# Optimization experiments

Hardware: AMD Instinct MI355X
Metric: run time of the kernel (lower is better)

## Reference

```python
import jax, jax.numpy as jnp
import numpy as np

N_NODES = 100000
N_EDGES = 1600000
N_IN = 8
N_PRE = 32
C = 128
N_LAYERS = 8


def _lin(key, fan_in, fan_out):
    kw, kb = jax.random.split(key)
    s = 1.0 / np.sqrt(fan_in).astype(np.float32)
    W = jax.random.uniform(kw, (fan_in, fan_out), minval=-s, maxval=s, dtype=jnp.float32)
    b = jax.random.uniform(kb, (fan_out,), minval=-s, maxval=s, dtype=jnp.float32)
    return W, b


def setup_inputs() -> dict:
    key = jax.random.key(0)
    ks = jax.random.split(key, 9)
    x = jax.random.normal(ks[0], (N_NODES, N_IN), dtype=jnp.float32)
    edge_index = jax.random.randint(ks[1], (2, N_EDGES), 0, N_NODES, dtype=jnp.int32)
    Wp, bp = _lin(ks[2], N_IN, N_PRE)      # preproc
    W1, b1 = _lin(ks[3], N_PRE, C)         # fc_input_1 (node_identity)
    W2, b2 = _lin(ks[4], N_PRE, C)         # fc_input_2
    Wg, bg = _lin(ks[5], C, C)             # tied GCNConv weight/bias
    Wd, bd = _lin(ks[6], 2 * C, C)         # tied dense fusion
    Wf1, bf1 = _lin(ks[7], 2 * C, C)       # final_fc1
    Wf2, bf2 = _lin(ks[8], C, 2)           # final_fc2
    return {"x": x, "edge_index": edge_index, "Wp": Wp, "bp": bp, "W1": W1, "b1": b1,
            "W2": W2, "b2": b2, "Wg": Wg, "bg": bg, "Wd": Wd, "bd": bd,
            "Wf1": Wf1, "bf1": bf1, "Wf2": Wf2, "bf2": bf2}


def _gcn(h, Wg, bg, src, dst):
    # PyG GCNConv: add self-loops, norm = deg^-1/2[src] * deg^-1/2[dst].
    # Norm factorizes, so scale at node level instead of per edge.
    hw = h @ Wg                                                  # [N, C]
    deg = jnp.zeros((N_NODES,), jnp.float32).at[dst].add(1.0) + 1.0  # +1 self-loop
    dis = jax.lax.rsqrt(deg)                                     # deg^-1/2
    hs = hw * dis[:, None]
    agg = jax.ops.segment_sum(hs[src], dst, num_segments=N_NODES)
    return (agg + hs) * dis[:, None] + bg                        # hs term = self-loop (deg^-1 * hw)


def reference(x, edge_index, Wp, bp, W1, b1, W2, b2, Wg, bg, Wd, bd, Wf1, bf1, Wf2, bf2):
    src, dst = edge_index[0], edge_index[1]
    h0 = x @ Wp + bp                       # preproc_activation = none
    ni = jax.nn.relu(h0 @ W1 + b1)         # node_identity
    h = jax.nn.relu(h0 @ W2 + b2)
    for _ in range(N_LAYERS):              # tied gnn layers; dropout is identity (inference)
        g = jax.nn.relu(_gcn(h, Wg, bg, src, dst))
        h = jax.nn.relu(jnp.concatenate([ni, g], axis=1) @ Wd + bd)
    h = jax.nn.relu(jnp.concatenate([ni, h], axis=1) @ Wf1 + bf1)
    return h @ Wf2 + bf2                   # output_activation never applied in forward
```

## Files before the change

### kernel.cpp

```cpp
#include <hip/hip_runtime.h>

#define N_NODES 100000
#define N_EDGES 1600000
#define NB 391
#define NTASK (N_NODES / 16)
#define COLPAD (N_EDGES + 7 * N_NODES + 64)

typedef unsigned short ushort_t;
typedef __attribute__((ext_vector_type(8))) short bf16x8;
typedef __attribute__((ext_vector_type(4))) float f32x4;

__device__ __forceinline__ float bf2f(unsigned short u) {
    union { unsigned u; float f; } x; x.u = ((unsigned)u) << 16; return x.f;
}
__device__ __forceinline__ unsigned short f2bf(float f) {
    union { float f; unsigned u; } x; x.f = f;
    unsigned r = x.u + 0x7fffu + ((x.u >> 16) & 1u);
    return (unsigned short)(r >> 16);
}

__global__ void k_zero(unsigned* p, int n) {
    int i = blockIdx.x * 256 + threadIdx.x;
    if (i < n) p[i] = 0u;
}

__global__ void k_filld(unsigned* p) {
    int i = blockIdx.x * 256 + threadIdx.x;
    if (i < COLPAD) p[i] = (unsigned)N_NODES;
}

__global__ void k_deg(const int* __restrict__ dst, unsigned* __restrict__ cnt) {
    int e = blockIdx.x * 256 + threadIdx.x;
    if (e < N_EDGES) atomicAdd(&cnt[dst[e]], 1u);
}

__global__ void k_dis(const unsigned* __restrict__ cnt, float* __restrict__ dis,
                      float* __restrict__ sdeg) {
    int i = blockIdx.x * 256 + threadIdx.x;
    if (i < N_NODES) {
        float d = (float)cnt[i] + 1.0f;
        float s = sqrtf(d);
        sdeg[i] = s;
        dis[i] = 1.0f / s;
    }
}

__global__ void __launch_bounds__(256) k_bsum(const unsigned* __restrict__ cnt,
                                              unsigned* __restrict__ bsum) {
    __shared__ unsigned sh[256];
    int i = blockIdx.x * 256 + threadIdx.x;
    sh[threadIdx.x] = (i < N_NODES) ? ((cnt[i] + 7u) & ~7u) : 0u;
    __syncthreads();
    for (int off = 128; off > 0; off >>= 1) {
        if (threadIdx.x < off) sh[threadIdx.x] += sh[threadIdx.x + off];
        __syncthreads();
    }
    if (threadIdx.x == 0) bsum[blockIdx.x] = sh[0];
}

__global__ void __launch_bounds__(512) k_bscan(unsigned* __restrict__ bsum) {
    __shared__ unsigned sh[512];
    int t = threadIdx.x;
    unsigned v = (t < NB) ? bsum[t] : 0u;
    sh[t] = v;
    __syncthreads();
    for (int off = 1; off < 512; off <<= 1) {
        unsigned u = (t >= off) ? sh[t - off] : 0u;
        __syncthreads();
        sh[t] += u;
        __syncthreads();
    }
    if (t < NB) bsum[t] = sh[t] - v;
}

__global__ void __launch_bounds__(256) k_apply(const unsigned* __restrict__ cnt,
                                               const unsigned* __restrict__ bsum,
                                               unsigned* __restrict__ prow,
                                               unsigned* __restrict__ cur) {
    __shared__ unsigned sh[256];
    int i = blockIdx.x * 256 + threadIdx.x;
    int t = threadIdx.x;
    unsigned v = (i < N_NODES) ? ((cnt[i] + 7u) & ~7u) : 0u;
    sh[t] = v;
    __syncthreads();
    for (int off = 1; off < 256; off <<= 1) {
        unsigned u = (t >= off) ? sh[t - off] : 0u;
        __syncthreads();
        sh[t] += u;
        __syncthreads();
    }
    if (i < N_NODES) {
        prow[i] = bsum[blockIdx.x] + sh[t] - v;
        cur[i] = 0u;
    }
    if (i == N_NODES - 1) prow[N_NODES] = bsum[blockIdx.x] + sh[t];
}

__global__ void k_fill(const int* __restrict__ src, const int* __restrict__ dst,
                       const unsigned* __restrict__ prow, unsigned* __restrict__ cur,
                       unsigned* __restrict__ colp) {
    int e = blockIdx.x * 256 + threadIdx.x;
    if (e < N_EDGES) {
        int d = dst[e];
        unsigned pos = prow[d] + atomicAdd(&cur[d], 1u);
        colp[pos] = (unsigned)src[e];
    }
}

__global__ void __launch_bounds__(256) k_sort(const unsigned* __restrict__ prow,
                                              unsigned* __restrict__ colp) {
    int i = blockIdx.x * 256 + threadIdx.x;
    if (i >= N_NODES) return;
    unsigned b = prow[i], e = prow[i + 1];
    for (unsigned j = b + 1; j < e; ++j) {
        unsigned v = colp[j];
        unsigned k = j;
        while (k > b && colp[k - 1] > v) { colp[k] = colp[k - 1]; --k; }
        colp[k] = v;
    }
}

__global__ void k_dummy(ushort_t* hdA, ushort_t* hdB) {
    int t = threadIdx.x;
    if (t < 128) hdA[(size_t)N_NODES * 128 + t] = 0;
    else hdB[(size_t)N_NODES * 128 + (t - 128)] = 0;
}

__global__ void k_tr(const float* __restrict__ Wd, const float* __restrict__ Wf1,
                     const float* __restrict__ Wg, ushort_t* __restrict__ WT) {
    const float* srcs[5] = {Wd, Wf1, Wg, Wd + 128 * 128, Wf1 + 128 * 128};
    const float* S = srcs[blockIdx.x];
    ushort_t* Dhi = WT + (size_t)(2 * blockIdx.x) * 16384;
    ushort_t* Dlo = Dhi + 16384;
    for (int i = threadIdx.x; i < 128 * 128; i += blockDim.x) {
        int n = i >> 7, k = i & 127;
        float w = S[k * 128 + n];
        unsigned short h = f2bf(w);
        Dhi[n * 128 + k] = h;
        Dlo[n * 128 + k] = f2bf(w - bf2f(h));
    }
}

__global__ void __launch_bounds__(128) k_pre1(
    const float* __restrict__ x, const float* __restrict__ Wp,
    const float* __restrict__ bp, const float* __restrict__ W1,
    const float* __restrict__ b1, const float* __restrict__ W2,
    const float* __restrict__ b2, const float* __restrict__ dis,
    ushort_t* __restrict__ ni, ushort_t* __restrict__ hd) {
    __shared__ float h0s[4][32];
    int j = threadIdx.x;
    long n0 = (long)blockIdx.x * 4;
    {
        int nn = j >> 5, c = j & 31;
        float acc = bp[c];
#pragma unroll
        for (int k = 0; k < 8; ++k)
            acc += x[(n0 + nn) * 8 + k] * Wp[k * 32 + c];
        h0s[nn][c] = acc;
    }
    __syncthreads();
    float ni_a[4], h1_a[4];
    float bb1 = b1[j], bb2 = b2[j];
#pragma unroll
    for (int m = 0; m < 4; ++m) { ni_a[m] = bb1; h1_a[m] = bb2; }
    for (int cc = 0; cc < 32; ++cc) {
        float w1 = W1[cc * 128 + j];
        float w2 = W2[cc * 128 + j];
#pragma unroll
        for (int m = 0; m < 4; ++m) {
            float h0v = h0s[m][cc];
            ni_a[m] += h0v * w1;
            h1_a[m] += h0v * w2;
        }
    }
#pragma unroll
    for (int m = 0; m < 4; ++m) {
        long node = n0 + m;
        ni[node * 128 + j] = f2bf(fmaxf(ni_a[m], 0.f));
        hd[node * 128 + j] = f2bf(fmaxf(h1_a[m], 0.f) * dis[node]);
    }
}

__device__ __forceinline__ void load_split_frags(const float* __restrict__ p,
                                                 bf16x8* ahi, bf16x8* alo) {
#pragma unroll
    for (int kc = 0; kc < 4; ++kc) {
        const float* q = p + kc * 32;
#pragma unroll
        for (int j = 0; j < 8; ++j) {
            float f = q[j];
            unsigned short h = f2bf(f);
            ahi[kc][j] = (short)h;
            alo[kc][j] = (short)f2bf(f - bf2f(h));
        }
    }
}

__device__ __forceinline__ void mfma_tiles(const bf16x8* ahi, const bf16x8* alo,
                                           const ushort_t* __restrict__ WThi,
                                           const ushort_t* __restrict__ WTlo,
                                           int r16, int q, f32x4* acc) {
#pragma unroll
    for (int t = 0; t < 8; ++t) {
        const ushort_t* bh = WThi + (t * 16 + r16) * 128 + q * 8;
        const ushort_t* bl = WTlo + (t * 16 + r16) * 128 + q * 8;
#pragma unroll
        for (int kc = 0; kc < 4; ++kc) {
            bf16x8 bhv = *(const bf16x8*)(bh + kc * 32);
            bf16x8 blv = *(const bf16x8*)(bl + kc * 32);
            acc[t] = __builtin_amdgcn_mfma_f32_16x16x32_bf16(alo[kc], bhv, acc[t], 0, 0, 0);
            acc[t] = __builtin_amdgcn_mfma_f32_16x16x32_bf16(ahi[kc], blv, acc[t], 0, 0, 0);
            acc[t] = __builtin_amdgcn_mfma_f32_16x16x32_bf16(ahi[kc], bhv, acc[t], 0, 0, 0);
        }
    }
}

__global__ void __launch_bounds__(256) k_niw(
    const ushort_t* __restrict__ in,
    const ushort_t* __restrict__ hiA, const ushort_t* __restrict__ loA,
    const float* __restrict__ biasA, ushort_t* __restrict__ outA,
    const ushort_t* __restrict__ hiB, const ushort_t* __restrict__ loB,
    const float* __restrict__ biasB, ushort_t* __restrict__ outB) {
    int task = blockIdx.x * 4 + (threadIdx.x >> 6);
    if (task >= NTASK) return;
    int lane = threadIdx.x & 63;
    int q = lane >> 4, r16 = lane & 15;
    long base = (long)task * 16;

    bf16x8 a[4];
    const ushort_t* arow = in + (base + r16) * 128 + q * 8;
#pragma unroll
    for (int kc = 0; kc < 4; ++kc) a[kc] = *(const bf16x8*)(arow + kc * 32);

    f32x4 accA[8], accB[8];
#pragma unroll
    for (int t = 0; t < 8; ++t) { accA[t] = {0.f, 0.f, 0.f, 0.f}; accB[t] = {0.f, 0.f, 0.f, 0.f}; }
#pragma unroll
    for (int t = 0; t < 8; ++t) {
        const ushort_t* bhA = hiA + (t * 16 + r16) * 128 + q * 8;
        const ushort_t* blA = loA + (t * 16 + r16) * 128 + q * 8;
        const ushort_t* bhB = hiB + (t * 16 + r16) * 128 + q * 8;
        const ushort_t* blB = loB + (t * 16 + r16) * 128 + q * 8;
#pragma unroll
        for (int kc = 0; kc < 4; ++kc) {
            accA[t] = __builtin_amdgcn_mfma_f32_16x16x32_bf16(a[kc], *(const bf16x8*)(blA + kc * 32), accA[t], 0, 0, 0);
            accA[t] = __builtin_amdgcn_mfma_f32_16x16x32_bf16(a[kc], *(const bf16x8*)(bhA + kc * 32), accA[t], 0, 0, 0);
            accB[t] = __builtin_amdgcn_mfma_f32_16x16x32_bf16(a[kc], *(const bf16x8*)(blB + kc * 32), accB[t], 0, 0, 0);
            accB[t] = __builtin_amdgcn_mfma_f32_16x16x32_bf16(a[kc], *(const bf16x8*)(bhB + kc * 32), accB[t], 0, 0, 0);
        }
    }
#pragma unroll
    for (int t = 0; t < 8; ++t) {
        int n = t * 16 + r16;
        float bvA = biasA[n], bvB = biasB[n];
#pragma unroll
        for (int r = 0; r < 4; ++r) {
            long node = base + q * 4 + r;
            outA[node * 128 + n] = f2bf(accA[t][r] + bvA);
            outB[node * 128 + n] = f2bf(accB[t][r] + bvB);
        }
    }
}

__device__ __forceinline__ void acc8(uint4 w, float* a) {
    a[0] += __uint_as_float(w.x << 16);
    a[1] += __uint_as_float(w.x & 0xffff0000u);
    a[2] += __uint_as_float(w.y << 16);
    a[3] += __uint_as_float(w.y & 0xffff0000u);
    a[4] += __uint_as_float(w.z << 16);
    a[5] += __uint_as_float(w.z & 0xffff0000u);
    a[6] += __uint_as_float(w.w << 16);
    a[7] += __uint_as_float(w.w & 0xffff0000u);
}

__device__ __forceinline__ void gather8(uint4* G, uint4 c0, uint4 c1,
                                        const uint4* __restrict__ h4, int l) {
    G[0] = h4[(long)c0.x * 16 + l];
    G[1] = h4[(long)c0.y * 16 + l];
    G[2] = h4[(long)c0.z * 16 + l];
    G[3] = h4[(long)c0.w * 16 + l];
    G[4] = h4[(long)c1.x * 16 + l];
    G[5] = h4[(long)c1.y * 16 + l];
    G[6] = h4[(long)c1.z * 16 + l];
    G[7] = h4[(long)c1.w * 16 + l];
}

__device__ __forceinline__ void accbatch(const uint4* G, float* a) {
#pragma unroll
    for (int j = 0; j < 8; ++j) acc8(G[j], a);
}

__global__ void __launch_bounds__(256, 4) k_fused(
    const unsigned* __restrict__ prow, const unsigned* __restrict__ colp,
    const ushort_t* __restrict__ hd_in,
    const ushort_t* __restrict__ hi_wg, const ushort_t* __restrict__ lo_wg,
    const float* __restrict__ bg,
    const ushort_t* __restrict__ hi_wd, const ushort_t* __restrict__ lo_wd,
    const ushort_t* __restrict__ niWd, const float* __restrict__ dis,
    ushort_t* __restrict__ hd_out) {
    __shared__ float gsh[4][16 * 132];
    int wid = threadIdx.x >> 6;
    int lane = threadIdx.x & 63;
    int task = blockIdx.x * 4 + wid;
    if (task >= NTASK) return;
    long base = (long)task * 16;
    float* gw = gsh[wid];
    const uint4* h4 = (const uint4*)hd_in;

    int g = lane >> 4;
    int l = lane & 15;

#pragma unroll 1
    for (int i = 0; i < 4; ++i) {
        int m = g * 4 + i;
        long node = base + m;
        float a[8] = {0.f, 0.f, 0.f, 0.f, 0.f, 0.f, 0.f, 0.f};
        uint4 own = h4[node * 16 + l];
        unsigned t0 = prow[node];
        int nb = (int)((prow[node + 1] - t0) >> 3);
        acc8(own, a);
        if (nb > 0) {
            const uint4* cp = (const uint4*)(colp + t0);
            uint4 cX0 = cp[0], cX1 = cp[1];
            uint4 cY0 = cp[2], cY1 = cp[3];
            cp += 4;
            uint4 GA[8], GB[8];
            gather8(GA, cX0, cX1, h4, l);
            int k = 0;
            for (; k + 2 < nb; k += 2) {
                cX0 = cp[0]; cX1 = cp[1];
                gather8(GB, cY0, cY1, h4, l);
                accbatch(GA, a);
                cY0 = cp[2]; cY1 = cp[3];
                cp += 4;
                gather8(GA, cX0, cX1, h4, l);
                accbatch(GB, a);
            }
            if (nb - k == 2) {
                gather8(GB, cY0, cY1, h4, l);
                accbatch(GA, a);
                accbatch(GB, a);
            } else {
                accbatch(GA, a);
            }
        }
        float* dstp = gw + m * 132 + 8 * l;
        *(float4*)dstp = make_float4(a[0], a[1], a[2], a[3]);
        *(float4*)(dstp + 4) = make_float4(a[4], a[5], a[6], a[7]);
    }

    int q = lane >> 4, r16 = lane & 15;
    bf16x8 ahi[4], alo[4];
    load_split_frags(gw + r16 * 132 + q * 8, ahi, alo);

    f32x4 acc[8];
#pragma unroll
    for (int t = 0; t < 8; ++t) acc[t] = {0.f, 0.f, 0.f, 0.f};
    mfma_tiles(ahi, alo, hi_wg, lo_wg, r16, q, acc);

    float sc[4];
#pragma unroll
    for (int r = 0; r < 4; ++r) sc[r] = dis[base + q * 4 + r];

#pragma unroll
    for (int t = 0; t < 8; ++t) {
        int n = t * 16 + r16;
        float bv = bg[n];
#pragma unroll
        for (int r = 0; r < 4; ++r) {
            int m = q * 4 + r;
            gw[m * 132 + n] = fmaxf(acc[t][r] * sc[r] + bv, 0.f);
        }
    }

    load_split_frags(gw + r16 * 132 + q * 8, ahi, alo);
#pragma unroll
    for (int t = 0; t < 8; ++t) acc[t] = {0.f, 0.f, 0.f, 0.f};
    mfma_tiles(ahi, alo, hi_wd, lo_wd, r16, q, acc);

#pragma unroll
    for (int t = 0; t < 8; ++t) {
        int n = t * 16 + r16;
#pragma unroll
        for (int r = 0; r < 4; ++r) {
            long node = base + q * 4 + r;
            float nv = bf2f(niWd[node * 128 + n]);
            hd_out[node * 128 + n] = f2bf(fmaxf(acc[t][r] + nv, 0.f) * sc[r]);
        }
    }
}

__global__ void __launch_bounds__(256) k_fin(
    const ushort_t* __restrict__ in, const ushort_t* __restrict__ WThi,
    const ushort_t* __restrict__ WTlo, const ushort_t* __restrict__ niWf,
    const float* __restrict__ sdeg, float* __restrict__ out) {
    int task = blockIdx.x * 4 + (threadIdx.x >> 6);
    if (task >= NTASK) return;
    int lane = threadIdx.x & 63;
    int q = lane >> 4, r16 = lane & 15;
    long base = (long)task * 16;

    bf16x8 a[4];
    const ushort_t* arow = in + (base + r16) * 128 + q * 8;
#pragma unroll
    for (int kc = 0; kc < 4; ++kc) a[kc] = *(const bf16x8*)(arow + kc * 32);

    f32x4 acc[8];
#pragma unroll
    for (int t = 0; t < 8; ++t) acc[t] = {0.f, 0.f, 0.f, 0.f};
#pragma unroll
    for (int t = 0; t < 8; ++t) {
        const ushort_t* bh = WThi + (t * 16 + r16) * 128 + q * 8;
        const ushort_t* bl = WTlo + (t * 16 + r16) * 128 + q * 8;
#pragma unroll
        for (int kc = 0; kc < 4; ++kc) {
            bf16x8 bhv = *(const bf16x8*)(bh + kc * 32);
            bf16x8 blv = *(const bf16x8*)(bl + kc * 32);
            acc[t] = __builtin_amdgcn_mfma_f32_16x16x32_bf16(a[kc], blv, acc[t], 0, 0, 0);
            acc[t] = __builtin_amdgcn_mfma_f32_16x16x32_bf16(a[kc], bhv, acc[t], 0, 0, 0);
        }
    }

    float sc[4];
#pragma unroll
    for (int r = 0; r < 4; ++r) sc[r] = sdeg[base + q * 4 + r];
#pragma unroll
    for (int t = 0; t < 8; ++t) {
        int n = t * 16 + r16;
#pragma unroll
        for (int r = 0; r < 4; ++r) {
            long node = base + q * 4 + r;
            float nv = bf2f(niWf[node * 128 + n]);
            out[node * 128 + n] = fmaxf(acc[t][r] * sc[r] + nv, 0.f);
        }
    }
}

__global__ void __launch_bounds__(256) k_fc2(const float* __restrict__ hf,
                                             const float* __restrict__ Wf2,
                                             const float* __restrict__ bf2v,
                                             float* __restrict__ out) {
    int node = blockIdx.x * 4 + (threadIdx.x >> 6);
    if (node >= N_NODES) return;
    int lane = threadIdx.x & 63;
    float2 hv = ((const float2*)hf)[(long)node * 64 + lane];
    float4 wv = *(const float4*)(Wf2 + lane * 4);
    float p0 = hv.x * wv.x + hv.y * wv.z;
    float p1 = hv.x * wv.y + hv.y * wv.w;
    for (int o = 32; o > 0; o >>= 1) {
        p0 += __shfl_down(p0, o, 64);
        p1 += __shfl_down(p1, o, 64);
    }
    if (lane == 0) {
        float2 r; r.x = p0 + bf2v[0]; r.y = p1 + bf2v[1];
        ((float2*)out)[node] = r;
    }
}

extern "C" void kernel_launch(void* const* d_in, const int* in_sizes, int n_in,
                              void* d_out, int out_size, void* d_ws, size_t ws_size,
                              hipStream_t stream) {
    const float* x    = (const float*)d_in[0];
    const int* ei     = (const int*)d_in[1];
    const float* Wp   = (const float*)d_in[2];
    const float* bp   = (const float*)d_in[3];
    const float* W1   = (const float*)d_in[4];
    const float* b1   = (const float*)d_in[5];
    const float* W2   = (const float*)d_in[6];
    const float* b2   = (const float*)d_in[7];
    const float* Wg   = (const float*)d_in[8];
    const float* bg   = (const float*)d_in[9];
    const float* Wd   = (const float*)d_in[10];
    const float* bd   = (const float*)d_in[11];
    const float* Wf1  = (const float*)d_in[12];
    const float* bf1  = (const float*)d_in[13];
    const float* Wf2  = (const float*)d_in[14];
    const float* bf2v = (const float*)d_in[15];

    char* w = (char*)d_ws;
    auto carve = [&](size_t bytes) {
        void* p = (void*)w;
        w += (bytes + 255) & ~(size_t)255;
        return p;
    };
    float* dis      = (float*)carve((size_t)N_NODES * 4);
    float* sdeg     = (float*)carve((size_t)N_NODES * 4);
    unsigned* cnt   = (unsigned*)carve((size_t)N_NODES * 4);
    unsigned* bsum  = (unsigned*)carve((size_t)NB * 4);
    unsigned* prow  = (unsigned*)carve((size_t)(N_NODES + 1) * 4);
    unsigned* colp  = (unsigned*)carve((size_t)COLPAD * 4);
    ushort_t* hdA   = (ushort_t*)carve((size_t)(N_NODES + 1) * 128 * 2);
    ushort_t* hdB   = (ushort_t*)carve((size_t)(N_NODES + 1) * 128 * 2);
    ushort_t* niB   = (ushort_t*)carve((size_t)N_NODES * 128 * 2);
    float* hf       = (float*)carve((size_t)N_NODES * 128 * 4);
    ushort_t* niWd  = (ushort_t*)carve((size_t)N_NODES * 128 * 2);
    ushort_t* niWf  = (ushort_t*)carve((size_t)N_NODES * 128 * 2);
    ushort_t* WT    = (ushort_t*)carve((size_t)10 * 16384 * 2);
    ushort_t* hi_wdtop  = WT + 0 * 16384; ushort_t* lo_wdtop  = WT + 1 * 16384;
    ushort_t* hi_wf1top = WT + 2 * 16384; ushort_t* lo_wf1top = WT + 3 * 16384;
    ushort_t* hi_wg     = WT + 4 * 16384; ushort_t* lo_wg     = WT + 5 * 16384;
    ushort_t* hi_wdbot  = WT + 6 * 16384; ushort_t* lo_wdbot  = WT + 7 * 16384;
    ushort_t* hi_wf1bot = WT + 8 * 16384; ushort_t* lo_wf1bot = WT + 9 * 16384;

    const int* srcp = ei;
    const int* dstp = ei + N_EDGES;

    const int GE = (N_EDGES + 255) / 256;
    const int GN = (N_NODES + 255) / 256;
    const int GP = (COLPAD + 255) / 256;
    const int GW = (N_NODES + 3) / 4;
    const int GG = (NTASK + 3) / 4;

    k_zero<<<GN, 256, 0, stream>>>(cnt, N_NODES);
    k_filld<<<GP, 256, 0, stream>>>(colp);
    k_deg<<<GE, 256, 0, stream>>>(dstp, cnt);
    k_dis<<<GN, 256, 0, stream>>>(cnt, dis, sdeg);
    k_bsum<<<NB, 256, 0, stream>>>(cnt, bsum);
    k_bscan<<<1, 512, 0, stream>>>(bsum);
    k_apply<<<NB, 256, 0, stream>>>(cnt, bsum, prow, cnt);
    k_fill<<<GE, 256, 0, stream>>>(srcp, dstp, prow, cnt, colp);
    k_sort<<<GN, 256, 0, stream>>>(prow, colp);
    k_dummy<<<1, 256, 0, stream>>>(hdA, hdB);
    k_tr<<<5, 256, 0, stream>>>(Wd, Wf1, Wg, WT);
    k_pre1<<<N_NODES / 4, 128, 0, stream>>>(x, Wp, bp, W1, b1, W2, b2, dis, niB, hdA);
    k_niw<<<GG, 256, 0, stream>>>(niB, hi_wdtop, lo_wdtop, bd, niWd,
                                  hi_wf1top, lo_wf1top, bf1, niWf);
    ushort_t* hin = hdA;
    ushort_t* hout = hdB;
    for (int l = 0; l < 8; ++l) {
        k_fused<<<GG, 256, 0, stream>>>(prow, colp, hin, hi_wg, lo_wg, bg,
                                        hi_wdbot, lo_wdbot, niWd, dis, hout);
        ushort_t* tmp = hin; hin = hout; hout = tmp;
    }
    k_fin<<<GG, 256, 0, stream>>>(hin, hi_wf1bot, lo_wf1bot, niWf, sdeg, hf);
    k_fc2<<<GW, 256, 0, stream>>>(hf, Wf2, bf2v, (float*)d_out);
}
```

Before: 1.886 ms.

## Fuse setup kernels, drop neighbor sort, fold final fc2 into fc1 epilogue

Merges the zero, fill and dummy kernels into one init kernel, folds the degree-norm computation into the block-sum kernel, and replaces the separate block-scan kernel with a per-block prefix reduction inside k_apply. It removes the per-row insertion sort of CSR column indices, and fuses the final 128->2 projection into the fc1 epilogue using shuffles, which removes the fp32 hidden buffer round-trip. This cuts launch count and memory traffic. Dropping the sort makes the neighbor order, and so the summation order, depend on atomic timing, which can change results slightly between runs and may lower gather locality.

Result: faster. 1.760 ms, median of 2 (-6.7%).

```diff
diff --git a/kernel.cpp b/kernel.cpp
--- a/kernel.cpp
+++ b/kernel.cpp
@@ -19,14 +19,15 @@
     return (unsigned short)(r >> 16);
 }
 
-__global__ void k_zero(unsigned* p, int n) {
+__global__ void k_init(unsigned* __restrict__ colp, unsigned* __restrict__ cnt,
+                       ushort_t* __restrict__ hdA, ushort_t* __restrict__ hdB) {
     int i = blockIdx.x * 256 + threadIdx.x;
-    if (i < n) p[i] = 0u;
-}
-
-__global__ void k_filld(unsigned* p) {
-    int i = blockIdx.x * 256 + threadIdx.x;
-    if (i < COLPAD) p[i] = (unsigned)N_NODES;
+    if (i < COLPAD) colp[i] = (unsigned)N_NODES;
+    if (i < N_NODES) cnt[i] = 0u;
+    if (i < 128) {
+        hdA[(size_t)N_NODES * 128 + i] = 0;
+        hdB[(size_t)N_NODES * 128 + i] = 0;
+    }
 }
 
 __global__ void k_deg(const int* __restrict__ dst, unsigned* __restrict__ cnt) {
@@ -34,43 +35,26 @@
     if (e < N_EDGES) atomicAdd(&cnt[dst[e]], 1u);
 }
 
-__global__ void k_dis(const unsigned* __restrict__ cnt, float* __restrict__ dis,
-                      float* __restrict__ sdeg) {
+__global__ void __launch_bounds__(256) k_bsum(const unsigned* __restrict__ cnt,
+                                              unsigned* __restrict__ bsum,
+                                              float* __restrict__ dis,
+                                              float* __restrict__ sdeg) {
+    __shared__ unsigned sh[256];
     int i = blockIdx.x * 256 + threadIdx.x;
+    unsigned c = (i < N_NODES) ? cnt[i] : 0u;
     if (i < N_NODES) {
-        float d = (float)cnt[i] + 1.0f;
+        float d = (float)c + 1.0f;
         float s = sqrtf(d);
         sdeg[i] = s;
         dis[i] = 1.0f / s;
     }
-}
-
-__global__ void __launch_bounds__(256) k_bsum(const unsigned* __restrict__ cnt,
-                                              unsigned* __restrict__ bsum) {
-    __shared__ unsigned sh[256];
-    int i = blockIdx.x * 256 + threadIdx.x;
-    sh[threadIdx.x] = (i < N_NODES) ? ((cnt[i] + 7u) & ~7u) : 0u;
+    sh[threadIdx.x] = (i < N_NODES) ? ((c + 7u) & ~7u) : 0u;
     __syncthreads();
     for (int off = 128; off > 0; off >>= 1) {
         if (threadIdx.x < off) sh[threadIdx.x] += sh[threadIdx.x + off];
         __syncthreads();
     }
     if (threadIdx.x == 0) bsum[blockIdx.x] = sh[0];
-}
-
-__global__ void __launch_bounds__(512) k_bscan(unsigned* __restrict__ bsum) {
-    __shared__ unsigned sh[512];
-    int t = threadIdx.x;
-    unsigned v = (t < NB) ? bsum[t] : 0u;
-    sh[t] = v;
-    __syncthreads();
-    for (int off = 1; off < 512; off <<= 1) {
-        unsigned u = (t >= off) ? sh[t - off] : 0u;
-        __syncthreads();
-        sh[t] += u;
-        __syncthreads();
-    }
-    if (t < NB) bsum[t] = sh[t] - v;
 }
 
 __global__ void __launch_bounds__(256) k_apply(const unsigned* __restrict__ cnt,
@@ -78,8 +62,19 @@
                                                unsigned* __restrict__ prow,
                                                unsigned* __restrict__ cur) {
     __shared__ unsigned sh[256];
+    __shared__ unsigned red[256];
     int i = blockIdx.x * 256 + threadIdx.x;
     int t = threadIdx.x;
+    unsigned s = 0;
+    for (int j = t; j < NB; j += 256)
+        if (j < blockIdx.x) s += bsum[j];
+    red[t] = s;
+    __syncthreads();
+    for (int off = 128; off > 0; off >>= 1) {
+        if (t < off) red[t] += red[t + off];
+        __syncthreads();
+    }
+    unsigned pre = red[0];
     unsigned v = (i < N_NODES) ? ((cnt[i] + 7u) & ~7u) : 0u;
     sh[t] = v;
     __syncthreads();
@@ -90,10 +85,10 @@
         __syncthreads();
     }
     if (i < N_NODES) {
-        prow[i] = bsum[blockIdx.x] + sh[t] - v;
+        prow[i] = pre + sh[t] - v;
         cur[i] = 0u;
     }
-    if (i == N_NODES - 1) prow[N_NODES] = bsum[blockIdx.x] + sh[t];
+    if (i == N_NODES - 1) prow[N_NODES] = pre + sh[t];
 }
 
 __global__ void k_fill(const int* __restrict__ src, const int* __restrict__ dst,
@@ -105,25 +100,6 @@
         unsigned pos = prow[d] + atomicAdd(&cur[d], 1u);
         colp[pos] = (unsigned)src[e];
     }
-}
-
-__global__ void __launch_bounds__(256) k_sort(const unsigned* __restrict__ prow,
-                                              unsigned* __restrict__ colp) {
-    int i = blockIdx.x * 256 + threadIdx.x;
-    if (i >= N_NODES) return;
-    unsigned b = prow[i], e = prow[i + 1];
-    for (unsigned j = b + 1; j < e; ++j) {
-        unsigned v = colp[j];
-        unsigned k = j;
-        while (k > b && colp[k - 1] > v) { colp[k] = colp[k - 1]; --k; }
-        colp[k] = v;
-    }
-}
-
-__global__ void k_dummy(ushort_t* hdA, ushort_t* hdB) {
-    int t = threadIdx.x;
-    if (t < 128) hdA[(size_t)N_NODES * 128 + t] = 0;
-    else hdB[(size_t)N_NODES * 128 + (t - 128)] = 0;
 }
 
 __global__ void k_tr(const float* __restrict__ Wd, const float* __restrict__ Wf1,
@@ -390,10 +366,11 @@
     }
 }
 
-__global__ void __launch_bounds__(256) k_fin(
+__global__ void __launch_bounds__(256) k_final(
     const ushort_t* __restrict__ in, const ushort_t* __restrict__ WThi,
     const ushort_t* __restrict__ WTlo, const ushort_t* __restrict__ niWf,
-    const float* __restrict__ sdeg, float* __restrict__ out) {
+    const float* __restrict__ sdeg, const float* __restrict__ Wf2,
+    const float* __restrict__ bf2v, float* __restrict__ out) {
     int task = blockIdx.x * 4 + (threadIdx.x >> 6);
     if (task >= NTASK) return;
     int lane = threadIdx.x & 63;
@@ -424,36 +401,36 @@
     float sc[4];
 #pragma unroll
     for (int r = 0; r < 4; ++r) sc[r] = sdeg[base + q * 4 + r];
+
+    float p0[4] = {0.f, 0.f, 0.f, 0.f}, p1[4] = {0.f, 0.f, 0.f, 0.f};
 #pragma unroll
     for (int t = 0; t < 8; ++t) {
         int n = t * 16 + r16;
+        float2 w2 = ((const float2*)Wf2)[n];
 #pragma unroll
         for (int r = 0; r < 4; ++r) {
             long node = base + q * 4 + r;
-            float nv = bf2f(niWf[node * 128 + n]);
-            out[node * 128 + n] = fmaxf(acc[t][r] * sc[r] + nv, 0.f);
-        }
-    }
-}
-
-__global__ void __launch_bounds__(256) k_fc2(const float* __restrict__ hf,
-                                             const float* __restrict__ Wf2,
-                                             const float* __restrict__ bf2v,
-                                             float* __restrict__ out) {
-    int node = blockIdx.x * 4 + (threadIdx.x >> 6);
-    if (node >= N_NODES) return;
-    int lane = threadIdx.x & 63;
-    float2 hv = ((const float2*)hf)[(long)node * 64 + lane];
-    float4 wv = *(const float4*)(Wf2 + lane * 4);
-    float p0 = hv.x * wv.x + hv.y * wv.z;
-    float p1 = hv.x * wv.y + hv.y * wv.w;
-    for (int o = 32; o > 0; o >>= 1) {
-        p0 += __shfl_down(p0, o, 64);
-        p1 += __shfl_down(p1, o, 64);
-    }
-    if (lane == 0) {
-        float2 r; r.x = p0 + bf2v[0]; r.y = p1 + bf2v[1];
-        ((float2*)out)[node] = r;
+            float v = fmaxf(acc[t][r] * sc[r] + bf2f(niWf[node * 128 + n]), 0.f);
+            p0[r] += v * w2.x;
+            p1[r] += v * w2.y;
+        }
+    }
+#pragma unroll
+    for (int step = 1; step < 16; step <<= 1) {
+#pragma unroll
+        for (int r = 0; r < 4; ++r) {
+            p0[r] += __shfl_xor(p0[r], step, 64);
+            p1[r] += __shfl_xor(p1[r], step, 64);
+        }
+    }
+    if (r16 == 0) {
+        float b0 = bf2v[0], b1v = bf2v[1];
+#pragma unroll
+        for (int r = 0; r < 4; ++r) {
+            long node = base + q * 4 + r;
+            float2 o; o.x = p0[r] + b0; o.y = p1[r] + b1v;
+            ((float2*)out)[node] = o;
+        }
     }
 }
 
@@ -492,7 +469,6 @@
     ushort_t* hdA   = (ushort_t*)carve((size_t)(N_NODES + 1) * 128 * 2);
     ushort_t* hdB   = (ushort_t*)carve((size_t)(N_NODES + 1) * 128 * 2);
     ushort_t* niB   = (ushort_t*)carve((size_t)N_NODES * 128 * 2);
-    float* hf       = (float*)carve((size_t)N_NODES * 128 * 4);
     ushort_t* niWd  = (ushort_t*)carve((size_t)N_NODES * 128 * 2);
     ushort_t* niWf  = (ushort_t*)carve((size_t)N_NODES * 128 * 2);
     ushort_t* WT    = (ushort_t*)carve((size_t)10 * 16384 * 2);
@@ -506,21 +482,14 @@
     const int* dstp = ei + N_EDGES;
 
     const int GE = (N_EDGES + 255) / 256;
-    const int GN = (N_NODES + 255) / 256;
     const int GP = (COLPAD + 255) / 256;
-    const int GW = (N_NODES + 3) / 4;
     const int GG = (NTASK + 3) / 4;
 
-    k_zero<<<GN, 256, 0, stream>>>(cnt, N_NODES);
-    k_filld<<<GP, 256, 0, stream>>>(colp);
+    k_init<<<GP, 256, 0, stream>>>(colp, cnt, hdA, hdB);
     k_deg<<<GE, 256, 0, stream>>>(dstp, cnt);
-    k_dis<<<GN, 256, 0, stream>>>(cnt, dis, sdeg);
-    k_bsum<<<NB, 256, 0, stream>>>(cnt, bsum);
-    k_bscan<<<1, 512, 0, stream>>>(bsum);
+    k_bsum<<<NB, 256, 0, stream>>>(cnt, bsum, dis, sdeg);
     k_apply<<<NB, 256, 0, stream>>>(cnt, bsum, prow, cnt);
     k_fill<<<GE, 256, 0, stream>>>(srcp, dstp, prow, cnt, colp);
-    k_sort<<<GN, 256, 0, stream>>>(prow, colp);
-    k_dummy<<<1, 256, 0, stream>>>(hdA, hdB);
     k_tr<<<5, 256, 0, stream>>>(Wd, Wf1, Wg, WT);
     k_pre1<<<N_NODES / 4, 128, 0, stream>>>(x, Wp, bp, W1, b1, W2, b2, dis, niB, hdA);
     k_niw<<<GG, 256, 0, stream>>>(niB, hi_wdtop, lo_wdtop, bd, niWd,
@@ -532,6 +501,6 @@
                                         hi_wdbot, lo_wdbot, niWd, dis, hout);
         ushort_t* tmp = hin; hin = hout; hout = tmp;
     }
-    k_fin<<<GG, 256, 0, stream>>>(hin, hi_wf1bot, lo_wf1bot, niWf, sdeg, hf);
-    k_fc2<<<GW, 256, 0, stream>>>(hf, Wf2, bf2v, (float*)d_out);
-}
+    k_final<<<GG, 256, 0, stream>>>(hin, hi_wf1bot, lo_wf1bot, niWf, sdeg,
+                                    Wf2, bf2v, (float*)d_out);
+}
```
